# Kernel optimization log

Hardware: AMD Instinct MI355X
Metric: run time of the kernel (lower is better)

Reference implementation:

```python
import jax, jax.numpy as jnp
import numpy as np
import math

DIM_T = 1024   # time-embedding dim == hidden_size (required for the code to run)
HID = 1024
IN = 1024
LAYERS = 4
N = 4096


def sinusoidal_pos_emb(t, dim):
    half = dim // 2
    freqs = jnp.exp(jnp.arange(half, dtype=jnp.float32) * (-math.log(10000.0) / (half - 1)))
    ang = t.astype(jnp.float32)[:, None] * freqs[None, :]  # (N, half)
    return jnp.concatenate([jnp.sin(ang), jnp.cos(ang)], axis=-1)  # (N, dim)


def setup_inputs() -> dict:
    key = jax.random.key(0)
    ks = jax.random.split(key, 16)
    s = 0.02
    inp = {
        "x": jax.random.normal(ks[0], (N, IN), jnp.float32),
        "timesteps": jax.random.randint(ks[1], (N,), 0, 1000, jnp.int32),
        "proj_w": jax.random.normal(ks[2], (DIM_T, IN), jnp.float32) * s,
        "proj_b": jnp.zeros((DIM_T,), jnp.float32),
        "te_w1": jax.random.normal(ks[3], (DIM_T, DIM_T), jnp.float32) * s,
        "te_b1": jnp.zeros((DIM_T,), jnp.float32),
        "te_w2": jax.random.normal(ks[4], (DIM_T, DIM_T), jnp.float32) * s,
        "te_b2": jnp.zeros((DIM_T,), jnp.float32),
        # all layers take dim_t-sized input (layer i>0 still consumes x[i] per the source)
        "Wih": jax.random.normal(ks[5], (LAYERS, 4 * HID, DIM_T), jnp.float32) * s,
        "Whh": jax.random.normal(ks[6], (LAYERS, 4 * HID, HID), jnp.float32) * s,
        "bih": jnp.zeros((LAYERS, 4 * HID), jnp.float32),
        "bhh": jnp.zeros((LAYERS, 4 * HID), jnp.float32),
        "lin_w": jax.random.normal(ks[7], (IN, HID), jnp.float32) * s,
        "lin_b": jnp.zeros((IN,), jnp.float32),
    }
    return inp


def _lstm_cell(xi, h, c, Wih, Whh, bih, bhh):
    g = Wih @ xi + bih + Whh @ h + bhh  # (4H,)
    i, f, gg, o = jnp.split(g, 4)
    c2 = jax.nn.sigmoid(f) * c + jax.nn.sigmoid(i) * jnp.tanh(gg)
    h2 = jax.nn.sigmoid(o) * jnp.tanh(c2)
    return h2, c2


def reference(x, timesteps, proj_w, proj_b, te_w1, te_b1, te_w2, te_b2,
              Wih, Whh, bih, bhh, lin_w, lin_b):
    emb = sinusoidal_pos_emb(timesteps, DIM_T)
    emb = jax.nn.silu(emb @ te_w1.T + te_b1) @ te_w2.T + te_b2  # (N, dim_t)
    xp = x @ proj_w.T + proj_b + emb  # (N, dim_t)

    def sample_step(carry, xi):
        def layer_step(hc, lp):
            h, c = hc
            W1, W2, b1, b2 = lp
            return _lstm_cell(xi, h, c, W1, W2, b1, b2), None
        carry, _ = jax.lax.scan(layer_step, carry, (Wih, Whh, bih, bhh))
        h, _ = carry
        return carry, lin_w @ h + lin_b

    h0 = jnp.zeros((HID,), jnp.float32)
    c0 = jnp.zeros((HID,), jnp.float32)
    _, outputs = jax.lax.scan(sample_step, (h0, c0), xp)  # (N, IN)
    return outputs
```

## Files before the change

### kernel.cpp

```cpp
#include <hip/hip_runtime.h>
#include <hip/hip_bf16.h>
#include <stdint.h>

#define NS 4096
#define DT 1024
#define H4 4096

__device__ __forceinline__ float sigm_f(float x) { return 1.f / (1.f + __expf(-x)); }
__device__ __forceinline__ float tanh_f(float x) {
    float ax = fminf(fabsf(x), 15.f);
    float t = 1.f - 2.f / (__expf(2.f * ax) + 1.f);
    return copysignf(t, x);
}

__global__ void emb_kernel(const int* __restrict__ ts, float* __restrict__ emb) {
    int t = blockIdx.x;
    int i = threadIdx.x;
    float tv = (float)ts[t];
    const float c = -0.018024149455922082f;
    float f = __expf(c * (float)i);
    float a = tv * f;
    float s, co;
    sincosf(a, &s, &co);
    emb[(size_t)t * DT + i] = s;
    emb[(size_t)t * DT + 512 + i] = co;
}

template <bool SILU, bool SKIP, int XGMODE>
__global__ __launch_bounds__(256) void gemm_bt(
    const float* __restrict__ A, const float* __restrict__ B,
    const float* __restrict__ bias, const float* __restrict__ bias2,
    const float* __restrict__ skip, float* __restrict__ Cf,
    __hip_bfloat16* __restrict__ Cb, int M, int Nc, int K)
{
    __shared__ __align__(16) float As[16][132];
    __shared__ __align__(16) float Bs[16][68];
    const int bn = blockIdx.x, bm = blockIdx.y, lz = blockIdx.z;
    if (XGMODE) {
        B     += (size_t)lz * H4 * DT;
        bias  += (size_t)lz * H4;
        bias2 += (size_t)lz * H4;
    }
    const int tid = threadIdx.x;
    const int tr = tid >> 4, tc = tid & 15;
    const int alr = tid >> 1, alc = (tid & 1) << 3;
    const int blr = tid >> 2, blc = (tid & 3) << 2;
    const float* Ap = A + (size_t)(bm * 128 + alr) * K + alc;
    const float* Bp = B + (size_t)(bn * 64 + blr) * K + blc;

    float acc[8][4];
#pragma unroll
    for (int i = 0; i < 8; i++)
#pragma unroll
        for (int j = 0; j < 4; j++) acc[i][j] = 0.f;

    for (int kk = 0; kk < K; kk += 16) {
        float4 a0 = *(const float4*)(Ap + kk);
        float4 a1 = *(const float4*)(Ap + kk + 4);
        float4 b0 = *(const float4*)(Bp + kk);
        __syncthreads();
        As[alc + 0][alr] = a0.x; As[alc + 1][alr] = a0.y;
        As[alc + 2][alr] = a0.z; As[alc + 3][alr] = a0.w;
        As[alc + 4][alr] = a1.x; As[alc + 5][alr] = a1.y;
        As[alc + 6][alr] = a1.z; As[alc + 7][alr] = a1.w;
        Bs[blc + 0][blr] = b0.x; Bs[blc + 1][blr] = b0.y;
        Bs[blc + 2][blr] = b0.z; Bs[blc + 3][blr] = b0.w;
        __syncthreads();
#pragma unroll
        for (int k = 0; k < 16; k++) {
            const float4 av0 = *(const float4*)&As[k][tr * 8];
            const float4 av1 = *(const float4*)&As[k][tr * 8 + 4];
            const float4 bv  = *(const float4*)&Bs[k][tc * 4];
            float aa[8] = {av0.x, av0.y, av0.z, av0.w, av1.x, av1.y, av1.z, av1.w};
            float bb[4] = {bv.x, bv.y, bv.z, bv.w};
#pragma unroll
            for (int i = 0; i < 8; i++)
#pragma unroll
                for (int j = 0; j < 4; j++)
                    acc[i][j] = fmaf(aa[i], bb[j], acc[i][j]);
        }
    }

#pragma unroll
    for (int i = 0; i < 8; i++) {
        int row = bm * 128 + tr * 8 + i;
#pragma unroll
        for (int j = 0; j < 4; j++) {
            int col = bn * 64 + tc * 4 + j;
            float v = acc[i][j] + bias[col];
            if (XGMODE) v += bias2[col];
            if (SKIP)   v += skip[(size_t)row * Nc + col];
            if (SILU)   v = v * (1.f / (1.f + __expf(-v)));
            if (XGMODE) {
                int q = col >> 10, jj = col & 1023;
                size_t idx = (size_t)row * 16384 + (size_t)lz * 4096
                           + ((size_t)(jj >> 2) << 4) + ((jj & 3) << 2) + q;
                if (XGMODE == 2) Cf[idx] = v;
                else             Cb[idx] = __float2bfloat16(v);
            } else {
                Cf[(size_t)row * Nc + col] = v;
            }
        }
    }
}

template <typename XT>
__global__ __launch_bounds__(256, 1) void seq_kernel(
    const float* __restrict__ Whh,
    const XT* __restrict__ XG,
    float* __restrict__ hall,
    uint64_t* hbuf)
{
    const int k = blockIdx.x;
    const int t = threadIdx.x;
    const int j = t & 15;
    const int cg = (t >> 4) & 3;
    const int w = t >> 6;
    const int q = j & 3, r = j >> 2;
    const int grow = q * 1024 + 4 * k + r;

    float wreg[4][64];
#pragma unroll
    for (int l = 0; l < 4; l++) {
        const float* src = Whh + ((size_t)l * H4 + grow) * 1024 + (w << 8) + (cg << 6);
#pragma unroll
        for (int i = 0; i < 16; i++) {
            int ii = (i + 4 * cg) & 15;
            float4 v = *(const float4*)(src + (ii << 2));
            wreg[l][i * 4 + 0] = v.x; wreg[l][i * 4 + 1] = v.y;
            wreg[l][i * 4 + 2] = v.z; wreg[l][i * 4 + 3] = v.w;
        }
    }

    __shared__ __align__(16) float lh[1024];
    __shared__ __align__(16) float lds_p[64];
    float creg = 0.f;

    for (int step = 0; step < NS; ++step) {
#pragma unroll
        for (int l = 0; l < 4; l++) {
            const int it = step * 4 + l + 1;
            const uint32_t rtag = (uint32_t)(it - 1);
            uint64_t* rb = (l & 1) ? (hbuf + 1024) : hbuf;
            uint64_t* wb = ((l + 1) & 1) ? (hbuf + 1024) : hbuf;

            float xg0 = 0.f, xg1 = 0.f, xg2 = 0.f, xg3 = 0.f;
            if (t < 4) {
                const XT* p = XG + (size_t)(it - 1) * H4 + (k << 4) + (t << 2);
                if constexpr (sizeof(XT) == 4) {
                    float4 v = *(const float4*)p;
                    xg0 = v.x; xg1 = v.y; xg2 = v.z; xg3 = v.w;
                } else {
                    ushort4 v = *(const ushort4*)p;
                    xg0 = __uint_as_float((uint32_t)v.x << 16);
                    xg1 = __uint_as_float((uint32_t)v.y << 16);
                    xg2 = __uint_as_float((uint32_t)v.z << 16);
                    xg3 = __uint_as_float((uint32_t)v.w << 16);
                }
            }

            uint32_t got = 0;
            while (got != 0xFu) {
#pragma unroll
                for (int m = 0; m < 4; m++) {
                    if (!(got & (1u << m))) {
                        uint64_t u = __hip_atomic_load(&rb[(m << 8) + t],
                                                       __ATOMIC_RELAXED, __HIP_MEMORY_SCOPE_AGENT);
                        if ((uint32_t)u == rtag) {
                            lh[(m << 8) + t] = __uint_as_float((uint32_t)(u >> 32));
                            got |= (1u << m);
                        }
                    }
                }
            }
            __syncthreads();

            const float* hbase = lh + (w << 8) + (cg << 6);
            float a0 = 0.f, a1 = 0.f, a2 = 0.f, a3 = 0.f;
#pragma unroll
            for (int i = 0; i < 16; i++) {
                int ii = (i + 4 * cg) & 15;
                const float4 hv = *(const float4*)(hbase + (ii << 2));
                a0 = fmaf(wreg[l][i * 4 + 0], hv.x, a0);
                a1 = fmaf(wreg[l][i * 4 + 1], hv.y, a1);
                a2 = fmaf(wreg[l][i * 4 + 2], hv.z, a2);
                a3 = fmaf(wreg[l][i * 4 + 3], hv.w, a3);
            }
            float acc = (a0 + a1) + (a2 + a3);
            acc += __shfl_xor(acc, 16);
            acc += __shfl_xor(acc, 32);
            if ((t & 63) < 16) lds_p[(j << 2) + w] = acc;
            __syncthreads();

            if (t < 4) {
                const float4 p0 = *(const float4*)&lds_p[(t << 4) + 0];
                const float4 p1 = *(const float4*)&lds_p[(t << 4) + 4];
                const float4 p2 = *(const float4*)&lds_p[(t << 4) + 8];
                const float4 p3 = *(const float4*)&lds_p[(t << 4) + 12];
                float gi = (p0.x + p0.y) + (p0.z + p0.w) + xg0;
                float gf = (p1.x + p1.y) + (p1.z + p1.w) + xg1;
                float gG = (p2.x + p2.y) + (p2.z + p2.w) + xg2;
                float go = (p3.x + p3.y) + (p3.z + p3.w) + xg3;
                float cn = sigm_f(gf) * creg + sigm_f(gi) * tanh_f(gG);
                creg = cn;
                float hn = sigm_f(go) * tanh_f(cn);
                if (l == 3) hall[(size_t)step * 1024 + (k << 2) + t] = hn;
                uint64_t word = ((uint64_t)__float_as_uint(hn) << 32) | (uint64_t)(uint32_t)it;
                __hip_atomic_store(&wb[(k << 2) + t], word,
                                   __ATOMIC_RELAXED, __HIP_MEMORY_SCOPE_AGENT);
            }
        }
    }
}

extern "C" void kernel_launch(void* const* d_in, const int* in_sizes, int n_in,
                              void* d_out, int out_size, void* d_ws, size_t ws_size,
                              hipStream_t stream)
{
    const float* x      = (const float*)d_in[0];
    const int*   ts     = (const int*)d_in[1];
    const float* proj_w = (const float*)d_in[2];
    const float* proj_b = (const float*)d_in[3];
    const float* te_w1  = (const float*)d_in[4];
    const float* te_b1  = (const float*)d_in[5];
    const float* te_w2  = (const float*)d_in[6];
    const float* te_b2  = (const float*)d_in[7];
    const float* Wih    = (const float*)d_in[8];
    const float* Whh    = (const float*)d_in[9];
    const float* bih    = (const float*)d_in[10];
    const float* bhh    = (const float*)d_in[11];
    const float* lin_w  = (const float*)d_in[12];
    const float* lin_b  = (const float*)d_in[13];
    float* out = (float*)d_out;

    char* ws = (char*)d_ws;
    const size_t MB16 = (size_t)NS * DT * 4;
    float* bufA = (float*)ws;
    float* bufB = (float*)(ws + MB16);
    const size_t xg_f32_bytes  = (size_t)NS * 16384 * 4;
    const size_t xg_bf16_bytes = (size_t)NS * 16384 * 2;
    const bool use_f32_xg = ws_size >= 2 * MB16 + xg_f32_bytes + 16384 + 64;
    float*          XGf = (float*)(ws + 2 * MB16);
    __hip_bfloat16* XGb = (__hip_bfloat16*)(ws + 2 * MB16);
    uint64_t* hbuf = (uint64_t*)(ws + 2 * MB16 +
                                 (use_f32_xg ? xg_f32_bytes : xg_bf16_bytes));

    hipMemsetAsync(hbuf, 0, 2 * 1024 * sizeof(uint64_t), stream);

    emb_kernel<<<NS, 512, 0, stream>>>(ts, bufA);
    gemm_bt<true, false, 0><<<dim3(16, 32), 256, 0, stream>>>(
        bufA, te_w1, te_b1, nullptr, nullptr, bufB, nullptr, NS, DT, DT);
    gemm_bt<false, false, 0><<<dim3(16, 32), 256, 0, stream>>>(
        bufB, te_w2, te_b2, nullptr, nullptr, bufA, nullptr, NS, DT, DT);
    gemm_bt<false, true, 0><<<dim3(16, 32), 256, 0, stream>>>(
        x, proj_w, proj_b, nullptr, bufA, bufB, nullptr, NS, DT, DT);
    if (use_f32_xg) {
        gemm_bt<false, false, 2><<<dim3(64, 32, 4), 256, 0, stream>>>(
            bufB, Wih, bih, bhh, nullptr, XGf, nullptr, NS, H4, DT);
        seq_kernel<float><<<256, 256, 0, stream>>>(Whh, XGf, bufA, hbuf);
    } else {
        gemm_bt<false, false, 1><<<dim3(64, 32, 4), 256, 0, stream>>>(
            bufB, Wih, bih, bhh, nullptr, nullptr, XGb, NS, H4, DT);
        seq_kernel<__hip_bfloat16><<<256, 256, 0, stream>>>(Whh, XGb, bufA, hbuf);
    }
    gemm_bt<false, false, 0><<<dim3(16, 32), 256, 0, stream>>>(
        bufA, lin_w, lin_b, nullptr, nullptr, out, nullptr, NS, DT, DT);
}
```

Baseline: 42.40 ms.

## Assign one wavefront per hidden row to drop second block barrier

The persistent LSTM sequence kernel now gives each wavefront one hidden unit (all four gate rows), so every lane holds a 64-column slice of all four gates. The dot product is reduced entirely with wave-level xor shuffles, and each wave computes its own cell update, which removes the LDS partial-sum buffer and the second __syncthreads per layer step. The shared h buffer is double-buffered so the next iteration's writes cannot race with reads of the current one. In exchange there are more shuffle rounds (six per gate) and every wave redundantly evaluates the activations and loads its own XG values.

```diff
diff --git a/kernel.cpp b/kernel.cpp
--- a/kernel.cpp
+++ b/kernel.cpp
@@ -113,27 +113,27 @@
 {
     const int k = blockIdx.x;
     const int t = threadIdx.x;
-    const int j = t & 15;
-    const int cg = (t >> 4) & 3;
     const int w = t >> 6;
-    const int q = j & 3, r = j >> 2;
-    const int grow = q * 1024 + 4 * k + r;
-
-    float wreg[4][64];
-#pragma unroll
-    for (int l = 0; l < 4; l++) {
-        const float* src = Whh + ((size_t)l * H4 + grow) * 1024 + (w << 8) + (cg << 6);
-#pragma unroll
-        for (int i = 0; i < 16; i++) {
-            int ii = (i + 4 * cg) & 15;
-            float4 v = *(const float4*)(src + (ii << 2));
-            wreg[l][i * 4 + 0] = v.x; wreg[l][i * 4 + 1] = v.y;
-            wreg[l][i * 4 + 2] = v.z; wreg[l][i * 4 + 3] = v.w;
-        }
-    }
-
-    __shared__ __align__(16) float lh[1024];
-    __shared__ __align__(16) float lds_p[64];
+    const int lam = t & 63;
+    const int row = (k << 2) + w;
+
+    float wreg[4][4][16];
+#pragma unroll
+    for (int l = 0; l < 4; l++)
+#pragma unroll
+        for (int q = 0; q < 4; q++) {
+            const float* src = Whh + ((size_t)l * H4 + q * 1024 + row) * 1024 + (lam << 2);
+#pragma unroll
+            for (int i = 0; i < 4; i++) {
+                float4 v = *(const float4*)(src + (i << 8));
+                wreg[l][q][i * 4 + 0] = v.x;
+                wreg[l][q][i * 4 + 1] = v.y;
+                wreg[l][q][i * 4 + 2] = v.z;
+                wreg[l][q][i * 4 + 3] = v.w;
+            }
+        }
+
+    __shared__ __align__(16) float lh[2][1024];
     float creg = 0.f;
 
     for (int step = 0; step < NS; ++step) {
@@ -141,12 +141,13 @@
         for (int l = 0; l < 4; l++) {
             const int it = step * 4 + l + 1;
             const uint32_t rtag = (uint32_t)(it - 1);
-            uint64_t* rb = (l & 1) ? (hbuf + 1024) : hbuf;
-            uint64_t* wb = ((l + 1) & 1) ? (hbuf + 1024) : hbuf;
-
-            float xg0 = 0.f, xg1 = 0.f, xg2 = 0.f, xg3 = 0.f;
-            if (t < 4) {
-                const XT* p = XG + (size_t)(it - 1) * H4 + (k << 4) + (t << 2);
+            uint64_t* rb = ((it - 1) & 1) ? (hbuf + 1024) : hbuf;
+            uint64_t* wb = (it & 1) ? (hbuf + 1024) : hbuf;
+            float* pb = lh[(it - 1) & 1];
+
+            float xg0, xg1, xg2, xg3;
+            {
+                const XT* p = XG + (size_t)(it - 1) * H4 + (k << 4) + (w << 2);
                 if constexpr (sizeof(XT) == 4) {
                     float4 v = *(const float4*)p;
                     xg0 = v.x; xg1 = v.y; xg2 = v.z; xg3 = v.w;
@@ -167,7 +168,7 @@
                         uint64_t u = __hip_atomic_load(&rb[(m << 8) + t],
                                                        __ATOMIC_RELAXED, __HIP_MEMORY_SCOPE_AGENT);
                         if ((uint32_t)u == rtag) {
-                            lh[(m << 8) + t] = __uint_as_float((uint32_t)(u >> 32));
+                            pb[(m << 8) + t] = __uint_as_float((uint32_t)(u >> 32));
                             got |= (1u << m);
                         }
                     }
@@ -175,38 +176,45 @@
             }
             __syncthreads();
 
-            const float* hbase = lh + (w << 8) + (cg << 6);
             float a0 = 0.f, a1 = 0.f, a2 = 0.f, a3 = 0.f;
 #pragma unroll
-            for (int i = 0; i < 16; i++) {
-                int ii = (i + 4 * cg) & 15;
-                const float4 hv = *(const float4*)(hbase + (ii << 2));
-                a0 = fmaf(wreg[l][i * 4 + 0], hv.x, a0);
-                a1 = fmaf(wreg[l][i * 4 + 1], hv.y, a1);
-                a2 = fmaf(wreg[l][i * 4 + 2], hv.z, a2);
-                a3 = fmaf(wreg[l][i * 4 + 3], hv.w, a3);
-            }
-            float acc = (a0 + a1) + (a2 + a3);
-            acc += __shfl_xor(acc, 16);
-            acc += __shfl_xor(acc, 32);
-            if ((t & 63) < 16) lds_p[(j << 2) + w] = acc;
-            __syncthreads();
-
-            if (t < 4) {
-                const float4 p0 = *(const float4*)&lds_p[(t << 4) + 0];
-                const float4 p1 = *(const float4*)&lds_p[(t << 4) + 4];
-                const float4 p2 = *(const float4*)&lds_p[(t << 4) + 8];
-                const float4 p3 = *(const float4*)&lds_p[(t << 4) + 12];
-                float gi = (p0.x + p0.y) + (p0.z + p0.w) + xg0;
-                float gf = (p1.x + p1.y) + (p1.z + p1.w) + xg1;
-                float gG = (p2.x + p2.y) + (p2.z + p2.w) + xg2;
-                float go = (p3.x + p3.y) + (p3.z + p3.w) + xg3;
-                float cn = sigm_f(gf) * creg + sigm_f(gi) * tanh_f(gG);
-                creg = cn;
-                float hn = sigm_f(go) * tanh_f(cn);
-                if (l == 3) hall[(size_t)step * 1024 + (k << 2) + t] = hn;
+            for (int i = 0; i < 4; i++) {
+                const float4 hv = *(const float4*)(pb + (i << 8) + (lam << 2));
+                a0 = fmaf(wreg[l][0][i * 4 + 0], hv.x, a0);
+                a0 = fmaf(wreg[l][0][i * 4 + 1], hv.y, a0);
+                a0 = fmaf(wreg[l][0][i * 4 + 2], hv.z, a0);
+                a0 = fmaf(wreg[l][0][i * 4 + 3], hv.w, a0);
+                a1 = fmaf(wreg[l][1][i * 4 + 0], hv.x, a1);
+                a1 = fmaf(wreg[l][1][i * 4 + 1], hv.y, a1);
+                a1 = fmaf(wreg[l][1][i * 4 + 2], hv.z, a1);
+                a1 = fmaf(wreg[l][1][i * 4 + 3], hv.w, a1);
+                a2 = fmaf(wreg[l][2][i * 4 + 0], hv.x, a2);
+                a2 = fmaf(wreg[l][2][i * 4 + 1], hv.y, a2);
+                a2 = fmaf(wreg[l][2][i * 4 + 2], hv.z, a2);
+                a2 = fmaf(wreg[l][2][i * 4 + 3], hv.w, a2);
+                a3 = fmaf(wreg[l][3][i * 4 + 0], hv.x, a3);
+                a3 = fmaf(wreg[l][3][i * 4 + 1], hv.y, a3);
+                a3 = fmaf(wreg[l][3][i * 4 + 2], hv.z, a3);
+                a3 = fmaf(wreg[l][3][i * 4 + 3], hv.w, a3);
+            }
+
+#pragma unroll
+            for (int s = 1; s < 64; s <<= 1) {
+                a0 += __shfl_xor(a0, s);
+                a1 += __shfl_xor(a1, s);
+                a2 += __shfl_xor(a2, s);
+                a3 += __shfl_xor(a3, s);
+            }
+
+            float gi = a0 + xg0, gf = a1 + xg1, gG = a2 + xg2, go = a3 + xg3;
+            float cn = sigm_f(gf) * creg + sigm_f(gi) * tanh_f(gG);
+            creg = cn;
+            float hn = sigm_f(go) * tanh_f(cn);
+
+            if (lam == 0) {
+                if (l == 3) hall[(size_t)step * 1024 + row] = hn;
                 uint64_t word = ((uint64_t)__float_as_uint(hn) << 32) | (uint64_t)(uint32_t)it;
-                __hip_atomic_store(&wb[(k << 2) + t], word,
+                __hip_atomic_store(&wb[row], word,
                                    __ATOMIC_RELAXED, __HIP_MEMORY_SCOPE_AGENT);
             }
         }
```

Measured after the change: 64.56 ms. 52.3% more time.
